# Kernel tuning notes

Measured on AMD Instinct MI355X. Metric: run time of the kernel, lower is better.

Reference implementation:

```python
import jax, jax.numpy as jnp
import numpy as np

B_, S_, D_ = 16, 2048, 256
H_ = 2 * D_          # S4D d_model = 2*hidden
NS = 64              # S4D state size (d_state)


def _layernorm(x, g, b, eps=1e-5):
    m = jnp.mean(x, axis=-1, keepdims=True)
    v = jnp.var(x, axis=-1, keepdims=True)
    return (x - m) * jax.lax.rsqrt(v + eps) * g + b


def setup_inputs() -> dict:
    key = jax.random.key(0)
    ks = jax.random.split(key, 12)
    x = jax.random.normal(ks[0], (B_, S_, D_), jnp.float32)
    # right-padded mask with varied lengths (signal: lengths = sum(mask), count_zeros = S - lengths)
    lengths = jax.random.randint(ks[1], (B_,), S_ // 2, S_ + 1)
    input_mask = (jnp.arange(S_)[None, :] < lengths[:, None]).astype(jnp.float32)
    # S4D (diag, diag-inv init, bilinear disc) parameters
    log_dt = jax.random.uniform(ks[2], (H_,), minval=jnp.log(1e-3), maxval=jnp.log(1e-1))
    log_A_real = jnp.log(0.5 * jnp.ones((H_, NS), jnp.float32))
    a_imag_row = (NS / jnp.pi) * (NS / (2.0 * jnp.arange(NS, dtype=jnp.float32) + 1.0) - 1.0)
    A_imag = jnp.broadcast_to(a_imag_row, (H_, NS)).copy()
    B_re = jnp.ones((H_, NS), jnp.float32)
    B_im = jnp.zeros((H_, NS), jnp.float32)
    C_re = jax.random.normal(ks[3], (H_, NS), jnp.float32) * (0.5 ** 0.5)
    C_im = jax.random.normal(ks[4], (H_, NS), jnp.float32) * (0.5 ** 0.5)
    D_skip = jax.random.normal(ks[5], (H_,), jnp.float32)
    # GLU: Linear(2D, 2D) then GLU -> D
    W_glu = jax.random.normal(ks[6], (2 * D_, 2 * D_), jnp.float32) / np.sqrt(2 * D_)
    b_glu = jnp.zeros((2 * D_,), jnp.float32)
    ln_gamma = jnp.ones((D_,), jnp.float32)
    ln_beta = jnp.zeros((D_,), jnp.float32)
    return {"input": x, "input_mask": input_mask, "log_dt": log_dt, "log_A_real": log_A_real,
            "A_imag": A_imag, "B_re": B_re, "B_im": B_im, "C_re": C_re, "C_im": C_im,
            "D_skip": D_skip, "W_glu": W_glu, "b_glu": b_glu, "ln_gamma": ln_gamma, "ln_beta": ln_beta}


def _s4d(z, log_dt, log_A_real, A_imag, B_re, B_im, C_re, C_im, D_skip):
    # z: [N, S, H] (transposed=False). Diagonal SSM, bilinear discretization, causal FFT conv.
    N, S, H = z.shape
    dt = jnp.exp(log_dt)[:, None]                        # [H,1]
    A = -jnp.exp(log_A_real) + 1j * A_imag               # [H,NS]
    Bc = B_re + 1j * B_im
    Cc = C_re + 1j * C_im
    dtA = dt * A
    dA = (1.0 + dtA / 2.0) / (1.0 - dtA / 2.0)           # bilinear
    Ct = Cc * Bc * dt / (1.0 - dtA / 2.0)                # folded B*C with bilinear dB factor
    # Vandermonde kernel K[h,l] = 2 Re sum_n Ct[h,n] * dA[h,n]^l
    vand = jnp.exp(jnp.log(dA)[:, :, None] * jnp.arange(S, dtype=jnp.float32))  # [H,NS,S] complex
    K = 2.0 * jnp.real(jnp.einsum('hn,hnl->hl', Ct, vand))                       # [H,S]
    L2 = 2 * S
    k_f = jnp.fft.rfft(K, n=L2)                          # [H, L2/2+1]
    x_f = jnp.fft.rfft(z, n=L2, axis=1)                  # [N, L2/2+1, H]
    y = jnp.fft.irfft(x_f * k_f.T[None], n=L2, axis=1)[:, :S, :]
    y = y + z * D_skip
    return jax.nn.gelu(y)                                # S4 block post-SSM activation; final_act=None, dropout=eval


def reference(input, input_mask, log_dt, log_A_real, A_imag, B_re, B_im, C_re, C_im,
              D_skip, W_glu, b_glu, ln_gamma, ln_beta):
    x = input
    N, S, D = x.shape
    res = x
    state = _layernorm(x, ln_gamma, ln_beta)             # prenorm=True
    count_zeros = jnp.sum(1.0 - input_mask, axis=1).astype(jnp.int32)   # [N]
    # reverse(state, cz): out[i] = state[(S-1-i-cz) mod S]  (flip then roll by count_zeros)
    rev_idx = (S - 1 - jnp.arange(S)[None, :] - count_zeros[:, None]) % S  # [N,S]
    reverse_bstate = jnp.take_along_axis(state, rev_idx[..., None], axis=1)
    z = jnp.concatenate([state, reverse_bstate], axis=-1)                 # [N,S,2D]
    z = _s4d(z, log_dt, log_A_real, A_imag, B_re, B_im, C_re, C_im, D_skip)
    fstate = z[..., :D]
    bstate = jnp.take_along_axis(z[..., D:], rev_idx[..., None], axis=1)  # reverse is an involution
    z = jnp.concatenate([fstate, bstate], axis=-1)                        # [N,S,2D]
    g = z @ W_glu + b_glu
    a, b = jnp.split(g, 2, axis=-1)
    out = a * jax.nn.sigmoid(b)                                           # GLU -> [N,S,D]
    out = out + res
    return out
```

## Files before the change

### kernel.cpp

```cpp
#include <hip/hip_runtime.h>
#include <hip/hip_bf16.h>
#include <math.h>

#define B_ 16
#define S_ 2048
#define D_ 256
#define H_ 512
#define NS_ 64
#define N2 4096
#define M_ (B_*S_)
#define XP(i) ((i) + ((i) >> 4))

typedef float f32x4 __attribute__((ext_vector_type(4)));
typedef short bf16x8 __attribute__((ext_vector_type(8)));

__device__ __forceinline__ unsigned short f2bf(float x) {
    __hip_bfloat16 h = __float2bfloat16(x);
    return *reinterpret_cast<unsigned short*>(&h);
}

__device__ __forceinline__ float gelu_f(float y) {
    float u = y + 0.044715f*y*y*y;
    return y / (1.0f + __builtin_exp2f(-2.3022082f * u));
}

template<bool INV>
__device__ __forceinline__ void dft16(float* xr, float* xi) {
    const float SGN = INV ? 1.0f : -1.0f;
    constexpr float W16R[4][4] = {
        {1.f, 1.f, 1.f, 1.f},
        {1.f,  0.92387953251128674f,  0.70710678118654757f,  0.38268343236508984f},
        {1.f,  0.70710678118654757f,  0.0f,                 -0.70710678118654746f},
        {1.f,  0.38268343236508984f, -0.70710678118654746f, -0.92387953251128674f}};
    constexpr float W16I[4][4] = {
        {0.f, 0.f, 0.f, 0.f},
        {0.f, -0.38268343236508978f, -0.70710678118654746f, -0.92387953251128674f},
        {0.f, -0.70710678118654746f, -1.0f,                 -0.70710678118654757f},
        {0.f, -0.92387953251128674f, -0.70710678118654757f,  0.38268343236508967f}};
    float tr[16], ti[16];
    #pragma unroll
    for (int n0 = 0; n0 < 4; ++n0) {
        float ar = xr[n0],    ai = xi[n0];
        float br = xr[n0+4],  bi = xi[n0+4];
        float cr = xr[n0+8],  ci = xi[n0+8];
        float dr = xr[n0+12], di = xi[n0+12];
        float sacr = ar+cr, saci = ai+ci;
        float dacr = ar-cr, daci = ai-ci;
        float sbdr = br+dr, sbdi = bi+di;
        float dbdr = br-dr, dbdi = bi-di;
        tr[0*4+n0] = sacr + sbdr;      ti[0*4+n0] = saci + sbdi;
        tr[2*4+n0] = sacr - sbdr;      ti[2*4+n0] = saci - sbdi;
        tr[1*4+n0] = dacr - SGN*dbdi;  ti[1*4+n0] = daci + SGN*dbdr;
        tr[3*4+n0] = dacr + SGN*dbdi;  ti[3*4+n0] = daci - SGN*dbdr;
    }
    #pragma unroll
    for (int kl = 1; kl < 4; ++kl) {
        #pragma unroll
        for (int n0 = 1; n0 < 4; ++n0) {
            float wr = W16R[kl][n0];
            float wi = INV ? -W16I[kl][n0] : W16I[kl][n0];
            float pr = tr[kl*4+n0], pi = ti[kl*4+n0];
            tr[kl*4+n0] = pr*wr - pi*wi;
            ti[kl*4+n0] = pr*wi + pi*wr;
        }
    }
    #pragma unroll
    for (int kl = 0; kl < 4; ++kl) {
        float ar = tr[kl*4+0], ai = ti[kl*4+0];
        float br = tr[kl*4+1], bi = ti[kl*4+1];
        float cr = tr[kl*4+2], ci = ti[kl*4+2];
        float dr = tr[kl*4+3], di = ti[kl*4+3];
        float sacr = ar+cr, saci = ai+ci;
        float dacr = ar-cr, daci = ai-ci;
        float sbdr = br+dr, sbdi = bi+di;
        float dbdr = br-dr, dbdi = bi-di;
        xr[kl+0]  = sacr + sbdr;      xi[kl+0]  = saci + sbdi;
        xr[kl+8]  = sacr - sbdr;      xi[kl+8]  = saci - sbdi;
        xr[kl+4]  = dacr - SGN*dbdi;  xi[kl+4]  = daci + SGN*dbdr;
        xr[kl+12] = dacr + SGN*dbdi;  xi[kl+12] = daci - SGN*dbdr;
    }
}

__device__ __forceinline__ void twiddle_recur(float* xr, float* xi, float w1r, float w1i) {
    float wr = w1r, wi = w1i;
    #pragma unroll
    for (int k = 1; k < 16; ++k) {
        float pr = xr[k], pi = xi[k];
        xr[k] = pr*wr - pi*wi;
        xi[k] = pr*wi + pi*wr;
        float nr = wr*w1r - wi*w1i;
        wi = wr*w1i + wi*w1r;
        wr = nr;
    }
}

__device__ __forceinline__ void fft4096_fwd_reg(float* xr, float* xi, float* lre, float* lim, int t) {
    dft16<false>(xr, xi);
    float w1r, w1i, ang;
    ang = (float)t * (-1.5339807878856412e-3f);
    sincosf(ang, &w1i, &w1r);
    twiddle_recur(xr, xi, w1r, w1i);
    #pragma unroll
    for (int k = 0; k < 16; ++k) { int idx = XP(k*256 + t); lre[idx] = xr[k]; lim[idx] = xi[k]; }
    __syncthreads();
    int k1 = t >> 4, n3 = t & 15;
    #pragma unroll
    for (int n2 = 0; n2 < 16; ++n2) {
        int idx = XP(k1*256 + n2*16 + n3);
        xr[n2] = lre[idx]; xi[n2] = lim[idx];
    }
    dft16<false>(xr, xi);
    ang = (float)n3 * (-2.4543692606170260e-2f);
    sincosf(ang, &w1i, &w1r);
    twiddle_recur(xr, xi, w1r, w1i);
    __syncthreads();
    #pragma unroll
    for (int k = 0; k < 16; ++k) { int idx = XP(k1*256 + k*16 + n3); lre[idx] = xr[k]; lim[idx] = xi[k]; }
    __syncthreads();
    int k2 = t & 15;
    #pragma unroll
    for (int n3b = 0; n3b < 16; ++n3b) {
        int idx = XP(k1*256 + k2*16 + n3b);
        xr[n3b] = lre[idx]; xi[n3b] = lim[idx];
    }
    dft16<false>(xr, xi);
}

__device__ __forceinline__ void fft4096_inv_reg(float* xr, float* xi, float* lre, float* lim, int t) {
    int k1 = t >> 4, k2 = t & 15;
    dft16<true>(xr, xi);
    float w1r, w1i, ang;
    ang = (float)k2 * (2.4543692606170260e-2f);
    sincosf(ang, &w1i, &w1r);
    twiddle_recur(xr, xi, w1r, w1i);
    __syncthreads();
    #pragma unroll
    for (int k = 0; k < 16; ++k) { int idx = XP(k1*256 + k2*16 + k); lre[idx] = xr[k]; lim[idx] = xi[k]; }
    __syncthreads();
    int n3 = t & 15;
    #pragma unroll
    for (int c = 0; c < 16; ++c) {
        int idx = XP(k1*256 + c*16 + n3);
        xr[c] = lre[idx]; xi[c] = lim[idx];
    }
    dft16<true>(xr, xi);
    __syncthreads();
    #pragma unroll
    for (int k = 0; k < 16; ++k) { int idx = XP(k1*256 + k*16 + n3); lre[idx] = xr[k]; lim[idx] = xi[k]; }
    __syncthreads();
    #pragma unroll
    for (int k = 0; k < 16; ++k) {
        int idx = XP(k*256 + t);
        xr[k] = lre[idx]; xi[k] = lim[idx];
    }
    ang = (float)t * (1.5339807878856412e-3f);
    sincosf(ang, &w1i, &w1r);
    twiddle_recur(xr, xi, w1r, w1i);
    dft16<true>(xr, xi);
}

__global__ void count_kernel(const float* __restrict__ mask, int* __restrict__ cz) {
    int b = blockIdx.x;
    int t = threadIdx.x;
    float s = 0.0f;
    for (int j = t; j < S_; j += 256) s += 1.0f - mask[b*S_ + j];
    for (int off = 32; off; off >>= 1) s += __shfl_xor(s, off);
    __shared__ float red[4];
    if ((t & 63) == 0) red[t >> 6] = s;
    __syncthreads();
    if (t == 0) {
        float tot = red[0] + red[1] + red[2] + red[3];
        cz[b] = (int)(tot + 0.5f);
    }
}

__global__ void wprep_kernel(const float* __restrict__ W, unsigned short* __restrict__ Wt) {
    int idx = blockIdx.x * 256 + threadIdx.x;
    int n = idx >> 9, k = idx & 511;
    Wt[idx] = f2bf(W[k*H_ + n]);
}

__global__ __launch_bounds__(256) void kfft_kernel(
        const float* __restrict__ log_dt, const float* __restrict__ log_A_real,
        const float* __restrict__ A_imag,
        const float* __restrict__ B_re, const float* __restrict__ B_im,
        const float* __restrict__ C_re, const float* __restrict__ C_im,
        float4* __restrict__ Kout) {
    int hp = blockIdx.x, t = threadIdx.x;
    int h0 = hp * 2;
    __shared__ float lre[N2 + N2/16];
    __shared__ float lim[N2 + N2/16];
    __shared__ float lnr[2][NS_], ctr[2][NS_], cti[2][NS_];
    __shared__ double th[2][NS_];

    if (t < 128) {
        int ch = t >> 6, n = t & 63, h = h0 + ch;
        float dt = expf(log_dt[h]);
        float Ar = -expf(log_A_real[h*NS_ + n]);
        float Ai = A_imag[h*NS_ + n];
        float drr = 1.0f - 0.5f*dt*Ar, dii = -0.5f*dt*Ai;
        float nr = 1.0f + 0.5f*dt*Ar, ni =  0.5f*dt*Ai;
        float den = drr*drr + dii*dii;
        float dAr = (nr*drr + ni*dii) / den;
        float dAi = (ni*drr - nr*dii) / den;
        float cr = C_re[h*NS_+n], ci = C_im[h*NS_+n];
        float br = B_re[h*NS_+n], bi = B_im[h*NS_+n];
        float pr = (cr*br - ci*bi) * dt, pi = (cr*bi + ci*br) * dt;
        float qr = (pr*drr + pi*dii) / den;
        float qi = (pi*drr - pr*dii) / den;
        lnr[ch][n] = 0.5f * logf(dAr*dAr + dAi*dAi);
        th[ch][n]  = atan2((double)dAi, (double)dAr);
        ctr[ch][n] = qr; cti[ch][n] = qi;
    }
    __syncthreads();

    float xr[16], xi[16];
    #pragma unroll
    for (int j = 0; j < 16; ++j) { xr[j] = 0.0f; xi[j] = 0.0f; }

    const double TWO_PI = 6.283185307179586;
    #pragma unroll
    for (int ch = 0; ch < 2; ++ch) {
        for (int n = 0; n < NS_; ++n) {
            float lr = lnr[ch][n];
            double thn = th[ch][n];
            double a0 = thn * (double)t;
            a0 -= floor(a0/TWO_PI + 0.5)*TWO_PI;
            float mb = expf(lr * (float)t);
            float sb, cb; sincosf((float)a0, &sb, &cb);
            float vr = mb*cb, vi = mb*sb;
            double as = thn * 256.0;
            as -= floor(as/TWO_PI + 0.5)*TWO_PI;
            float ms = expf(lr * 256.0f);
            float ss, cs; sincosf((float)as, &ss, &cs);
            float str = ms*cs, sti = ms*ss;
            float cr = ctr[ch][n], ci = cti[ch][n];
            #pragma unroll
            for (int j = 0; j < 8; ++j) {
                float contrib = cr*vr - ci*vi;
                if (ch == 0) xr[j] += contrib; else xi[j] += contrib;
                float nvr = vr*str - vi*sti;
                vi = vr*sti + vi*str;
                vr = nvr;
            }
        }
    }
    #pragma unroll
    for (int j = 0; j < 8; ++j) { xr[j] *= 2.0f; xi[j] *= 2.0f; }

    fft4096_fwd_reg(xr, xi, lre, lim, t);

    __syncthreads();
    #pragma unroll
    for (int k = 0; k < 16; ++k) { int idx = XP(k*256 + t); lre[idx] = xr[k]; lim[idx] = xi[k]; }
    __syncthreads();

    const float scale = 1.0f / (float)N2;
    #pragma unroll
    for (int it = 0; it < 16; ++it) {
        int j = 256*it + t;
        int k = (t >> 4) + ((t & 15) << 4) + (it << 8);
        int kc = (N2 - k) & (N2 - 1);
        int j2 = ((kc >> 8) << 8) + ((kc & 15) << 4) + ((kc >> 4) & 15);
        float za = xr[it], zb = xi[it];
        float zc = lre[XP(j2)], zd = lim[XP(j2)];
        float Xr = 0.5f*(za + zc), Xi2 = 0.5f*(zb - zd);
        float Yr = 0.5f*(zb + zd), Yi = 0.5f*(zc - za);
        Kout[(size_t)hp*N2 + j] = make_float4(Xr*scale, Xi2*scale, Yr*scale, Yi*scale);
    }
}

__global__ __launch_bounds__(256) void ln_kernel(
        const float* __restrict__ x, const float* __restrict__ gamma,
        const float* __restrict__ beta, const int* __restrict__ cz,
        float* __restrict__ z_t) {
    int blk = blockIdx.x;
    int b = blk >> 6;
    int s0 = (blk & 63) * 32;
    int t = threadIdx.x;
    int lane = t & 63, wave = t >> 6;
    __shared__ float st[32][257];

    float4 g4  = *(const float4*)(gamma + lane*4);
    float4 be4 = *(const float4*)(beta  + lane*4);
    for (int q = 0; q < 8; ++q) {
        int row = wave*8 + q;
        int s = s0 + row;
        float4 v = *(const float4*)(x + ((size_t)(b*S_ + s))*D_ + lane*4);
        float sum = v.x + v.y + v.z + v.w;
        float ss  = v.x*v.x + v.y*v.y + v.z*v.z + v.w*v.w;
        for (int off = 32; off; off >>= 1) {
            sum += __shfl_xor(sum, off);
            ss  += __shfl_xor(ss, off);
        }
        float mean = sum * (1.0f/(float)D_);
        float var  = ss  * (1.0f/(float)D_) - mean*mean;
        float rstd = rsqrtf(var + 1e-5f);
        st[row][lane*4+0] = (v.x - mean)*rstd*g4.x + be4.x;
        st[row][lane*4+1] = (v.y - mean)*rstd*g4.y + be4.y;
        st[row][lane*4+2] = (v.z - mean)*rstd*g4.z + be4.z;
        st[row][lane*4+3] = (v.w - mean)*rstd*g4.w + be4.w;
    }
    __syncthreads();
    int czb = cz[b];
    int s_off = t & 31, dg = t >> 5;
    int s = s0 + s_off;
    int bs = (2*S_ - 1 - czb - s) % S_;
    for (int i = 0; i < 32; ++i) {
        int d = dg + 8*i;
        float v = st[s_off][d];
        z_t[((size_t)(b*H_ + d      ))*S_ + s ] = v;
        z_t[((size_t)(b*H_ + D_ + d ))*S_ + bs] = v;
    }
}

__global__ __launch_bounds__(256) void fftconv_kernel(
        const float* __restrict__ z_t, const float4* __restrict__ Kf4,
        const float* __restrict__ D_skip, unsigned short* __restrict__ ybf) {
    int blk = blockIdx.x;
    int b  = blk >> 8;
    int hp = blk & 255;
    int h0 = hp * 2;
    int t = threadIdx.x;
    __shared__ float lre[N2 + N2/16];
    __shared__ float lim[N2 + N2/16];

    const float* zrow1 = z_t + ((size_t)(b*H_ + h0    ))*S_;
    const float* zrow2 = z_t + ((size_t)(b*H_ + h0 + 1))*S_;
    float xr[16], xi[16];
    float z1r[8], z2r[8];
    #pragma unroll
    for (int j = 0; j < 8; ++j) {
        int s = t + 256*j;
        float v1 = zrow1[s], v2 = zrow2[s];
        z1r[j] = v1; z2r[j] = v2;
        xr[j] = v1;  xi[j] = v2;
        xr[j+8] = 0.0f; xi[j+8] = 0.0f;
    }

    fft4096_fwd_reg(xr, xi, lre, lim, t);

    __syncthreads();
    #pragma unroll
    for (int k = 0; k < 16; ++k) { int idx = XP(k*256 + t); lre[idx] = xr[k]; lim[idx] = xi[k]; }
    __syncthreads();

    const float4* kp = Kf4 + (size_t)hp * N2;
    #pragma unroll
    for (int it = 0; it < 16; ++it) {
        int j = 256*it + t;
        int k = (t >> 4) + ((t & 15) << 4) + (it << 8);
        int kc = (N2 - k) & (N2 - 1);
        int j2 = ((kc >> 8) << 8) + ((kc & 15) << 4) + ((kc >> 4) & 15);
        float za = xr[it], zb = xi[it];
        float zc = lre[XP(j2)], zd = lim[XP(j2)];
        float Xr = 0.5f*(za + zc), Xi2 = 0.5f*(zb - zd);
        float Yr = 0.5f*(zb + zd), Yi = 0.5f*(zc - za);
        float4 kk = kp[j];
        float Pr = Xr*kk.x - Xi2*kk.y, Pi = Xr*kk.y + Xi2*kk.x;
        float Qr = Yr*kk.z - Yi*kk.w,  Qi = Yr*kk.w + Yi*kk.z;
        xr[it] = Pr - Qi;
        xi[it] = Pi + Qr;
    }

    fft4096_inv_reg(xr, xi, lre, lim, t);

    float dsk1 = D_skip[h0], dsk2 = D_skip[h0+1];
    unsigned short* yb1 = ybf + ((size_t)(b*H_ + h0    ))*2*S_;
    unsigned short* yb2 = ybf + ((size_t)(b*H_ + h0 + 1))*2*S_;
    #pragma unroll
    for (int j = 0; j < 8; ++j) {
        int s = t + 256*j;
        float y1 = xr[j] + dsk1 * z1r[j];
        float y2 = xi[j] + dsk2 * z2r[j];
        yb1[s] = f2bf(gelu_f(y1));
        yb2[s] = f2bf(gelu_f(y2));
    }
}

__global__ __launch_bounds__(256) void transpose_kernel(
        const unsigned short* __restrict__ ybf, const int* __restrict__ cz,
        unsigned short* __restrict__ A) {
    int b  = blockIdx.z;
    int h0 = blockIdx.y * 64;
    int s0 = blockIdx.x * 64;
    int t = threadIdx.x;
    int tx = t & 63, ty = t >> 6;
    __shared__ unsigned short tile[64][65];
    bool back = (h0 >= D_);
    int czb = cz[b];
    int s = s0 + tx;
    int scol = back ? ((2*S_ - 1 - czb - s) % S_) : s;
    for (int i = 0; i < 16; ++i) {
        int hh = ty*16 + i;
        tile[hh][tx] = ybf[((size_t)(b*H_ + h0 + hh))*2*S_ + scol];
    }
    __syncthreads();
    for (int i = 0; i < 16; ++i) {
        int sl = ty*16 + i;
        A[((size_t)(b*S_ + s0 + sl))*H_ + h0 + tx] = tile[tx][sl];
    }
}

__global__ __launch_bounds__(256) void glu_gemm_kernel(
        const unsigned short* __restrict__ A, const unsigned short* __restrict__ Wt,
        const float* __restrict__ bglu, const float* __restrict__ x,
        float* __restrict__ out) {
    int m0 = blockIdx.x * 64;
    int n0 = blockIdx.y * 64;
    int t = threadIdx.x;
    int lane = t & 63, w = t >> 6;
    int wm = w & 1, wgrp = w >> 1;
    __shared__ __align__(16) short As[64][40];
    __shared__ __align__(16) short Bs[2][64][40];
    __shared__ float gs[64][132];

    f32x4 acc[2][4];
    for (int mf = 0; mf < 2; ++mf)
        for (int nf = 0; nf < 4; ++nf)
            acc[mf][nf] = (f32x4){0.0f, 0.0f, 0.0f, 0.0f};

    int srow = t >> 2;
    int scol = (t & 3) * 8;
    for (int kk = 0; kk < H_; kk += 32) {
        __syncthreads();
        *(int4*)&As[srow][scol]    = *(const int4*)(A  + ((size_t)(m0 + srow))*H_ + kk + scol);
        *(int4*)&Bs[0][srow][scol] = *(const int4*)(Wt + ((size_t)(n0 + srow))*H_ + kk + scol);
        *(int4*)&Bs[1][srow][scol] = *(const int4*)(Wt + ((size_t)(n0 + 256 + srow))*H_ + kk + scol);
        __syncthreads();
        int lr = lane & 15, ks = (lane >> 4) * 8;
        bf16x8 af[2], bf[4];
        for (int mf = 0; mf < 2; ++mf)
            af[mf] = *(bf16x8*)&As[wm*32 + mf*16 + lr][ks];
        for (int nf = 0; nf < 4; ++nf)
            bf[nf] = *(bf16x8*)&Bs[wgrp][nf*16 + lr][ks];
        for (int mf = 0; mf < 2; ++mf)
            for (int nf = 0; nf < 4; ++nf)
                acc[mf][nf] = __builtin_amdgcn_mfma_f32_16x16x32_bf16(af[mf], bf[nf], acc[mf][nf], 0, 0, 0);
    }
    __syncthreads();
    for (int mf = 0; mf < 2; ++mf)
        for (int nf = 0; nf < 4; ++nf)
            for (int r = 0; r < 4; ++r) {
                int row = wm*32 + mf*16 + (lane >> 4)*4 + r;
                int col = wgrp*64 + nf*16 + (lane & 15);
                gs[row][col] = acc[mf][nf][r];
            }
    __syncthreads();
    int col = t & 63;
    float ba = bglu[n0 + col], bb = bglu[n0 + 256 + col];
    for (int i = 0; i < 16; ++i) {
        int row = (t >> 6)*16 + i;
        size_t mr = (size_t)(m0 + row);
        float av = gs[row][col]      + ba;
        float bv = gs[row][64 + col] + bb;
        float sig = 1.0f / (1.0f + expf(-bv));
        out[mr*D_ + n0 + col] = av*sig + x[mr*D_ + n0 + col];
    }
}

extern "C" void kernel_launch(void* const* d_in, const int* in_sizes, int n_in,
                              void* d_out, int out_size, void* d_ws, size_t ws_size,
                              hipStream_t stream) {
    const float* x         = (const float*)d_in[0];
    const float* mask      = (const float*)d_in[1];
    const float* log_dt    = (const float*)d_in[2];
    const float* log_A_real= (const float*)d_in[3];
    const float* A_imag    = (const float*)d_in[4];
    const float* B_re      = (const float*)d_in[5];
    const float* B_im      = (const float*)d_in[6];
    const float* C_re      = (const float*)d_in[7];
    const float* C_im      = (const float*)d_in[8];
    const float* D_skip    = (const float*)d_in[9];
    const float* W_glu     = (const float*)d_in[10];
    const float* b_glu     = (const float*)d_in[11];
    const float* ln_gamma  = (const float*)d_in[12];
    const float* ln_beta   = (const float*)d_in[13];
    float* out = (float*)d_out;

    char* ws = (char*)d_ws;
    int*            cz  = (int*)ws;
    float*          z_t = (float*)(ws + 256);
    float4*         Kf  = (float4*)(ws + 256 + 67108864);
    unsigned short* Abf = (unsigned short*)(ws + 256 + 67108864 + 16777216);
    unsigned short* Wt  = (unsigned short*)(ws + 256 + 67108864 + 16777216 + 33554432);
    unsigned short* ybf = (unsigned short*)z_t;

    count_kernel<<<B_, 256, 0, stream>>>(mask, cz);
    wprep_kernel<<<(H_*H_)/256, 256, 0, stream>>>(W_glu, Wt);
    kfft_kernel<<<H_/2, 256, 0, stream>>>(log_dt, log_A_real, A_imag, B_re, B_im, C_re, C_im, Kf);
    ln_kernel<<<B_*(S_/32), 256, 0, stream>>>(x, ln_gamma, ln_beta, cz, z_t);
    fftconv_kernel<<<B_*(H_/2), 256, 0, stream>>>(z_t, (const float4*)Kf, D_skip, ybf);
    transpose_kernel<<<dim3(S_/64, H_/64, B_), 256, 0, stream>>>(ybf, cz, Abf);
    glu_gemm_kernel<<<dim3(M_/64, D_/64), 256, 0, stream>>>(Abf, Wt, b_glu, x, out);
}
```

Measured before the change: 352.4 us.

## Rework GLU GEMM tiling with async LDS loads and cheapen FFT twiddles

The GLU GEMM now uses 128x256 tiles with double-buffered global_load_lds staging, an XOR-swizzled LDS layout, and an epilogue that applies bias, sigmoid and residual straight from registers instead of going through a shared-memory scratch tile. The FFT twiddles and the SSM kernel generation switch from sincosf and double-precision atan2 to hardware sin/cos in revolutions plus float exp2/log2. A precomputed per-state step is also stored in shared memory. dft16 gains modes that skip work for inputs known to be zero-padded (the first forward stage) and for outputs that are discarded (the last inverse stage). Together these target GEMM data movement and transcendental cost, at the risk of lower twiddle accuracy and much higher register pressure in the GEMM (32 accumulators per thread).

```diff
diff --git a/kernel.cpp b/kernel.cpp
--- a/kernel.cpp
+++ b/kernel.cpp
@@ -24,7 +24,10 @@
     return y / (1.0f + __builtin_exp2f(-2.3022082f * u));
 }
 
-template<bool INV>
+__device__ __forceinline__ float cos_rev(float r) { return __builtin_amdgcn_cosf(r); }
+__device__ __forceinline__ float sin_rev(float r) { return __builtin_amdgcn_sinf(r); }
+
+template<bool INV, int MODE>
 __device__ __forceinline__ void dft16(float* xr, float* xi) {
     const float SGN = INV ? 1.0f : -1.0f;
     constexpr float W16R[4][4] = {
@@ -40,18 +43,27 @@
     float tr[16], ti[16];
     #pragma unroll
     for (int n0 = 0; n0 < 4; ++n0) {
-        float ar = xr[n0],    ai = xi[n0];
-        float br = xr[n0+4],  bi = xi[n0+4];
-        float cr = xr[n0+8],  ci = xi[n0+8];
-        float dr = xr[n0+12], di = xi[n0+12];
-        float sacr = ar+cr, saci = ai+ci;
-        float dacr = ar-cr, daci = ai-ci;
-        float sbdr = br+dr, sbdi = bi+di;
-        float dbdr = br-dr, dbdi = bi-di;
-        tr[0*4+n0] = sacr + sbdr;      ti[0*4+n0] = saci + sbdi;
-        tr[2*4+n0] = sacr - sbdr;      ti[2*4+n0] = saci - sbdi;
-        tr[1*4+n0] = dacr - SGN*dbdi;  ti[1*4+n0] = daci + SGN*dbdr;
-        tr[3*4+n0] = dacr + SGN*dbdi;  ti[3*4+n0] = daci - SGN*dbdr;
+        if (MODE == 1) {
+            float ar = xr[n0],   ai = xi[n0];
+            float br = xr[n0+4], bi = xi[n0+4];
+            tr[0*4+n0] = ar + br;        ti[0*4+n0] = ai + bi;
+            tr[2*4+n0] = ar - br;        ti[2*4+n0] = ai - bi;
+            tr[1*4+n0] = ar - SGN*bi;    ti[1*4+n0] = ai + SGN*br;
+            tr[3*4+n0] = ar + SGN*bi;    ti[3*4+n0] = ai - SGN*br;
+        } else {
+            float ar = xr[n0],    ai = xi[n0];
+            float br = xr[n0+4],  bi = xi[n0+4];
+            float cr = xr[n0+8],  ci = xi[n0+8];
+            float dr = xr[n0+12], di = xi[n0+12];
+            float sacr = ar+cr, saci = ai+ci;
+            float dacr = ar-cr, daci = ai-ci;
+            float sbdr = br+dr, sbdi = bi+di;
+            float dbdr = br-dr, dbdi = bi-di;
+            tr[0*4+n0] = sacr + sbdr;      ti[0*4+n0] = saci + sbdi;
+            tr[2*4+n0] = sacr - sbdr;      ti[2*4+n0] = saci - sbdi;
+            tr[1*4+n0] = dacr - SGN*dbdi;  ti[1*4+n0] = daci + SGN*dbdr;
+            tr[3*4+n0] = dacr + SGN*dbdi;  ti[3*4+n0] = daci - SGN*dbdr;
+        }
     }
     #pragma unroll
     for (int kl = 1; kl < 4; ++kl) {
@@ -75,9 +87,11 @@
         float sbdr = br+dr, sbdi = bi+di;
         float dbdr = br-dr, dbdi = bi-di;
         xr[kl+0]  = sacr + sbdr;      xi[kl+0]  = saci + sbdi;
-        xr[kl+8]  = sacr - sbdr;      xi[kl+8]  = saci - sbdi;
         xr[kl+4]  = dacr - SGN*dbdi;  xi[kl+4]  = daci + SGN*dbdr;
-        xr[kl+12] = dacr + SGN*dbdi;  xi[kl+12] = daci - SGN*dbdr;
+        if (MODE != 2) {
+            xr[kl+8]  = sacr - sbdr;      xi[kl+8]  = saci - sbdi;
+            xr[kl+12] = dacr + SGN*dbdi;  xi[kl+12] = daci - SGN*dbdr;
+        }
     }
 }
 
@@ -95,10 +109,9 @@
 }
 
 __device__ __forceinline__ void fft4096_fwd_reg(float* xr, float* xi, float* lre, float* lim, int t) {
-    dft16<false>(xr, xi);
-    float w1r, w1i, ang;
-    ang = (float)t * (-1.5339807878856412e-3f);
-    sincosf(ang, &w1i, &w1r);
+    dft16<false, 1>(xr, xi);
+    float rv = (float)t * (1.0f/4096.0f);
+    float w1r = cos_rev(rv), w1i = -sin_rev(rv);
     twiddle_recur(xr, xi, w1r, w1i);
     #pragma unroll
     for (int k = 0; k < 16; ++k) { int idx = XP(k*256 + t); lre[idx] = xr[k]; lim[idx] = xi[k]; }
@@ -109,9 +122,9 @@
         int idx = XP(k1*256 + n2*16 + n3);
         xr[n2] = lre[idx]; xi[n2] = lim[idx];
     }
-    dft16<false>(xr, xi);
-    ang = (float)n3 * (-2.4543692606170260e-2f);
-    sincosf(ang, &w1i, &w1r);
+    dft16<false, 0>(xr, xi);
+    rv = (float)n3 * (1.0f/256.0f);
+    w1r = cos_rev(rv); w1i = -sin_rev(rv);
     twiddle_recur(xr, xi, w1r, w1i);
     __syncthreads();
     #pragma unroll
@@ -123,15 +136,14 @@
         int idx = XP(k1*256 + k2*16 + n3b);
         xr[n3b] = lre[idx]; xi[n3b] = lim[idx];
     }
-    dft16<false>(xr, xi);
+    dft16<false, 0>(xr, xi);
 }
 
 __device__ __forceinline__ void fft4096_inv_reg(float* xr, float* xi, float* lre, float* lim, int t) {
     int k1 = t >> 4, k2 = t & 15;
-    dft16<true>(xr, xi);
-    float w1r, w1i, ang;
-    ang = (float)k2 * (2.4543692606170260e-2f);
-    sincosf(ang, &w1i, &w1r);
+    dft16<true, 0>(xr, xi);
+    float rv = (float)k2 * (1.0f/256.0f);
+    float w1r = cos_rev(rv), w1i = sin_rev(rv);
     twiddle_recur(xr, xi, w1r, w1i);
     __syncthreads();
     #pragma unroll
@@ -143,7 +155,7 @@
         int idx = XP(k1*256 + c*16 + n3);
         xr[c] = lre[idx]; xi[c] = lim[idx];
     }
-    dft16<true>(xr, xi);
+    dft16<true, 0>(xr, xi);
     __syncthreads();
     #pragma unroll
     for (int k = 0; k < 16; ++k) { int idx = XP(k1*256 + k*16 + n3); lre[idx] = xr[k]; lim[idx] = xi[k]; }
@@ -153,10 +165,10 @@
         int idx = XP(k*256 + t);
         xr[k] = lre[idx]; xi[k] = lim[idx];
     }
-    ang = (float)t * (1.5339807878856412e-3f);
-    sincosf(ang, &w1i, &w1r);
+    rv = (float)t * (1.0f/4096.0f);
+    w1r = cos_rev(rv); w1i = sin_rev(rv);
     twiddle_recur(xr, xi, w1r, w1i);
-    dft16<true>(xr, xi);
+    dft16<true, 2>(xr, xi);
 }
 
 __global__ void count_kernel(const float* __restrict__ mask, int* __restrict__ cz) {
@@ -190,8 +202,8 @@
     int h0 = hp * 2;
     __shared__ float lre[N2 + N2/16];
     __shared__ float lim[N2 + N2/16];
-    __shared__ float lnr[2][NS_], ctr[2][NS_], cti[2][NS_];
-    __shared__ double th[2][NS_];
+    __shared__ float thrv[2][NS_], lnr2[2][NS_], ctr[2][NS_], cti[2][NS_];
+    __shared__ float stpr[2][NS_], stpi[2][NS_];
 
     if (t < 128) {
         int ch = t >> 6, n = t & 63, h = h0 + ch;
@@ -208,9 +220,14 @@
         float pr = (cr*br - ci*bi) * dt, pi = (cr*bi + ci*br) * dt;
         float qr = (pr*drr + pi*dii) / den;
         float qi = (pi*drr - pr*dii) / den;
-        lnr[ch][n] = 0.5f * logf(dAr*dAr + dAi*dAi);
-        th[ch][n]  = atan2((double)dAi, (double)dAr);
-        ctr[ch][n] = qr; cti[ch][n] = qi;
+        float trv = atan2f(dAi, dAr) * 0.15915494309189535f;
+        float l2  = 0.5f * log2f(dAr*dAr + dAi*dAi);
+        thrv[ch][n] = trv; lnr2[ch][n] = l2;
+        ctr[ch][n] = qr;   cti[ch][n] = qi;
+        float ms = __builtin_exp2f(l2 * 256.0f);
+        float rv = trv * 256.0f; rv -= floorf(rv);
+        stpr[ch][n] = ms * cos_rev(rv);
+        stpi[ch][n] = ms * sin_rev(rv);
     }
     __syncthreads();
 
@@ -218,29 +235,23 @@
     #pragma unroll
     for (int j = 0; j < 16; ++j) { xr[j] = 0.0f; xi[j] = 0.0f; }
 
-    const double TWO_PI = 6.283185307179586;
+    float tf = (float)t;
     #pragma unroll
     for (int ch = 0; ch < 2; ++ch) {
         for (int n = 0; n < NS_; ++n) {
-            float lr = lnr[ch][n];
-            double thn = th[ch][n];
-            double a0 = thn * (double)t;
-            a0 -= floor(a0/TWO_PI + 0.5)*TWO_PI;
-            float mb = expf(lr * (float)t);
-            float sb, cb; sincosf((float)a0, &sb, &cb);
-            float vr = mb*cb, vi = mb*sb;
-            double as = thn * 256.0;
-            as -= floor(as/TWO_PI + 0.5)*TWO_PI;
-            float ms = expf(lr * 256.0f);
-            float ss, cs; sincosf((float)as, &ss, &cs);
-            float str = ms*cs, sti = ms*ss;
-            float cr = ctr[ch][n], ci = cti[ch][n];
+            float trv = thrv[ch][n], l2 = lnr2[ch][n];
+            float f = trv * tf; f -= floorf(f);
+            float mag = __builtin_exp2f(l2 * tf);
+            float vr = mag * cos_rev(f);
+            float vi = mag * sin_rev(f);
+            float sr = stpr[ch][n], si = stpi[ch][n];
+            float cr = ctr[ch][n],  ci = cti[ch][n];
             #pragma unroll
             for (int j = 0; j < 8; ++j) {
                 float contrib = cr*vr - ci*vi;
                 if (ch == 0) xr[j] += contrib; else xi[j] += contrib;
-                float nvr = vr*str - vi*sti;
-                vi = vr*sti + vi*str;
+                float nvr = vr*sr - vi*si;
+                vi = vr*si + vi*sr;
                 vr = nvr;
             }
         }
@@ -406,56 +417,91 @@
         const unsigned short* __restrict__ A, const unsigned short* __restrict__ Wt,
         const float* __restrict__ bglu, const float* __restrict__ x,
         float* __restrict__ out) {
-    int m0 = blockIdx.x * 64;
-    int n0 = blockIdx.y * 64;
+    int m0 = blockIdx.x * 128;
+    int nh = blockIdx.y;
     int t = threadIdx.x;
     int lane = t & 63, w = t >> 6;
-    int wm = w & 1, wgrp = w >> 1;
-    __shared__ __align__(16) short As[64][40];
-    __shared__ __align__(16) short Bs[2][64][40];
-    __shared__ float gs[64][132];
-
-    f32x4 acc[2][4];
+    __shared__ __align__(16) unsigned short Ab[2][4096];
+    __shared__ __align__(16) unsigned short Bb[2][8192];
+
+    f32x4 acc[2][16];
+    #pragma unroll
     for (int mf = 0; mf < 2; ++mf)
-        for (int nf = 0; nf < 4; ++nf)
+        #pragma unroll
+        for (int nf = 0; nf < 16; ++nf)
             acc[mf][nf] = (f32x4){0.0f, 0.0f, 0.0f, 0.0f};
 
-    int srow = t >> 2;
-    int scol = (t & 3) * 8;
-    for (int kk = 0; kk < H_; kk += 32) {
+    int r = t >> 2;
+    int kch = (t & 3) * 8;
+    int wbase = (t >> 6) * 1024;
+
+    auto stage = [&](int buf, int kk) {
+        #pragma unroll
+        for (int i = 0; i < 2; ++i) {
+            int row = i*64 + r;
+            int kel = kch ^ (((row >> 2) & 3) << 3);
+            const unsigned short* src = A + ((size_t)(m0 + row))*H_ + kk + kel;
+            char* dst = (char*)&Ab[buf][0] + i*4096 + wbase;
+            __builtin_amdgcn_global_load_lds((const __attribute__((address_space(1))) void*)src,
+                                             (__attribute__((address_space(3))) void*)dst, 16, 0, 0);
+        }
+        #pragma unroll
+        for (int i = 0; i < 4; ++i) {
+            int rb = i*64 + r;
+            int n = nh*128 + rb + (rb & 128);
+            int kel = kch ^ (((rb >> 2) & 3) << 3);
+            const unsigned short* src = Wt + ((size_t)n)*H_ + kk + kel;
+            char* dst = (char*)&Bb[buf][0] + i*4096 + wbase;
+            __builtin_amdgcn_global_load_lds((const __attribute__((address_space(1))) void*)src,
+                                             (__attribute__((address_space(3))) void*)dst, 16, 0, 0);
+        }
+    };
+
+    int lr = lane & 15, ksel = lane >> 4;
+    stage(0, 0);
+    __syncthreads();
+
+    #pragma unroll 1
+    for (int step = 0; step < 16; ++step) {
+        int cur = step & 1;
+        if (step < 15) stage(cur ^ 1, (step + 1) * 32);
+        const char* pa = (const char*)&Ab[cur][0];
+        const char* pb = (const char*)&Bb[cur][0];
+        bf16x8 af[2];
+        #pragma unroll
+        for (int mf = 0; mf < 2; ++mf) {
+            int arow = w*32 + mf*16 + lr;
+            af[mf] = *(const bf16x8*)(pa + arow*64 + ((ksel*16) ^ (((arow >> 2) & 3) << 4)));
+        }
+        #pragma unroll
+        for (int nf = 0; nf < 16; ++nf) {
+            int brow = nf*16 + lr;
+            bf16x8 bv = *(const bf16x8*)(pb + brow*64 + ((ksel*16) ^ (((brow >> 2) & 3) << 4)));
+            acc[0][nf] = __builtin_amdgcn_mfma_f32_16x16x32_bf16(af[0], bv, acc[0][nf], 0, 0, 0);
+            acc[1][nf] = __builtin_amdgcn_mfma_f32_16x16x32_bf16(af[1], bv, acc[1][nf], 0, 0, 0);
+        }
         __syncthreads();
-        *(int4*)&As[srow][scol]    = *(const int4*)(A  + ((size_t)(m0 + srow))*H_ + kk + scol);
-        *(int4*)&Bs[0][srow][scol] = *(const int4*)(Wt + ((size_t)(n0 + srow))*H_ + kk + scol);
-        *(int4*)&Bs[1][srow][scol] = *(const int4*)(Wt + ((size_t)(n0 + 256 + srow))*H_ + kk + scol);
-        __syncthreads();
-        int lr = lane & 15, ks = (lane >> 4) * 8;
-        bf16x8 af[2], bf[4];
-        for (int mf = 0; mf < 2; ++mf)
-            af[mf] = *(bf16x8*)&As[wm*32 + mf*16 + lr][ks];
-        for (int nf = 0; nf < 4; ++nf)
-            bf[nf] = *(bf16x8*)&Bs[wgrp][nf*16 + lr][ks];
-        for (int mf = 0; mf < 2; ++mf)
-            for (int nf = 0; nf < 4; ++nf)
-                acc[mf][nf] = __builtin_amdgcn_mfma_f32_16x16x32_bf16(af[mf], bf[nf], acc[mf][nf], 0, 0, 0);
-    }
-    __syncthreads();
-    for (int mf = 0; mf < 2; ++mf)
-        for (int nf = 0; nf < 4; ++nf)
-            for (int r = 0; r < 4; ++r) {
-                int row = wm*32 + mf*16 + (lane >> 4)*4 + r;
-                int col = wgrp*64 + nf*16 + (lane & 15);
-                gs[row][col] = acc[mf][nf][r];
+    }
+
+    int r4 = (lane >> 4) * 4;
+    #pragma unroll
+    for (int mf = 0; mf < 2; ++mf) {
+        #pragma unroll
+        for (int nf = 0; nf < 8; ++nf) {
+            int tc = nf*16 + lr;
+            int dcol = nh*128 + tc;
+            float ba = bglu[dcol];
+            float bb = bglu[256 + dcol];
+            #pragma unroll
+            for (int rr = 0; rr < 4; ++rr) {
+                int row = w*32 + mf*16 + r4 + rr;
+                size_t mi = (size_t)(m0 + row);
+                float av = acc[mf][nf][rr] + ba;
+                float bv = acc[mf][nf+8][rr] + bb;
+                float sig = 1.0f / (1.0f + __builtin_exp2f(-1.4426950408889634f * bv));
+                out[mi*D_ + dcol] = av*sig + x[mi*D_ + dcol];
             }
-    __syncthreads();
-    int col = t & 63;
-    float ba = bglu[n0 + col], bb = bglu[n0 + 256 + col];
-    for (int i = 0; i < 16; ++i) {
-        int row = (t >> 6)*16 + i;
-        size_t mr = (size_t)(m0 + row);
-        float av = gs[row][col]      + ba;
-        float bv = gs[row][64 + col] + bb;
-        float sig = 1.0f / (1.0f + expf(-bv));
-        out[mr*D_ + n0 + col] = av*sig + x[mr*D_ + n0 + col];
+        }
     }
 }
 
@@ -492,5 +538,5 @@
     ln_kernel<<<B_*(S_/32), 256, 0, stream>>>(x, ln_gamma, ln_beta, cz, z_t);
     fftconv_kernel<<<B_*(H_/2), 256, 0, stream>>>(z_t, (const float4*)Kf, D_skip, ybf);
     transpose_kernel<<<dim3(S_/64, H_/64, B_), 256, 0, stream>>>(ybf, cz, Abf);
-    glu_gemm_kernel<<<dim3(M_/64, D_/64), 256, 0, stream>>>(Abf, Wt, b_glu, x, out);
-}
+    glu_gemm_kernel<<<dim3(M_/128, 2), 256, 0, stream>>>(Abf, Wt, b_glu, x, out);
+}
```

Result: faster. 299.8 us (-14.9%).
